# Kernel tuning notes

Measured on AMD Instinct MI355X. Metric: run time of the kernel, lower is better.

The kernel has to match this reference:

```python
import jax, jax.numpy as jnp
import numpy as np

V = 50257      # vocab size
H = 512        # hidden size
S = 128        # source length
BEAM = 5       # beam width (matches beam_width=5 default)
TMAX = 32      # MAX_LENGTH decode cap
SOS, EOS = 1, 2
NEG = -1e9


def setup_inputs() -> dict:
    key = jax.random.key(0)
    ks = jax.random.split(key, 12)
    p = lambda k, shape: jax.random.normal(k, shape, jnp.float32) * 0.02
    return {
        "input_tokens": jax.random.randint(ks[0], (S,), 0, V),
        "embedding": p(ks[1], (V, H)),
        "enc_Wih": p(ks[2], (3 * H, H)),
        "enc_Whh": p(ks[3], (3 * H, H)),
        "enc_bih": jnp.zeros((3 * H,), jnp.float32),
        "enc_bhh": jnp.zeros((3 * H,), jnp.float32),
        "dec_Wih": p(ks[4], (3 * H, H)),
        "dec_Whh": p(ks[5], (3 * H, H)),
        "dec_bih": jnp.zeros((3 * H,), jnp.float32),
        "dec_bhh": jnp.zeros((3 * H,), jnp.float32),
        "W_concat": p(ks[6], (2 * H, H)),
        "W_vocab": p(ks[7], (H, V)),
    }


def gru_cell(x, h, Wih, Whh, bih, bhh):
    # x, h: [..., H]
    gi = x @ Wih.T + bih
    gh = h @ Whh.T + bhh
    ir, iz, inn = jnp.split(gi, 3, -1)
    hr, hz, hn = jnp.split(gh, 3, -1)
    r = jax.nn.sigmoid(ir + hr)
    z = jax.nn.sigmoid(iz + hz)
    n = jnp.tanh(inn + r * hn)
    return (1.0 - z) * n + z * h


def reference(input_tokens, embedding, enc_Wih, enc_Whh, enc_bih, enc_bhh,
              dec_Wih, dec_Whh, dec_bih, dec_bhh, W_concat, W_vocab):
    # ---- encoder: 1-layer GRU over source tokens ----
    src_emb = embedding[input_tokens]                       # [S, H]

    def enc_step(h, x):
        h2 = gru_cell(x, h, enc_Wih, enc_Whh, enc_bih, enc_bhh)
        return h2, h2

    enc_h, enc_out = jax.lax.scan(enc_step, jnp.zeros((H,), src_emb.dtype), src_emb)
    # enc_out: [S, H], enc_h: [H]

    def decode_step(tokens, hidden):
        # tokens: [B] int, hidden: [B, H]
        x = embedding[tokens]                               # [B, H]
        h = gru_cell(x, hidden, dec_Wih, dec_Whh, dec_bih, dec_bhh)
        attn = jax.nn.softmax(h @ enc_out.T, axis=-1)       # [B, S] Luong dot attention
        ctx = attn @ enc_out                                # [B, H]
        o = jnp.tanh(jnp.concatenate([h, ctx], -1) @ W_concat)
        logp = jax.nn.log_softmax(o @ W_vocab, axis=-1)     # [B, V]
        return logp, h

    # ---- batched beam search (GPU-resident equivalent of the heapq loop) ----
    tokens0 = jnp.full((BEAM,), SOS, jnp.int32)
    hidden0 = jnp.tile(enc_h[None], (BEAM, 1))
    scores0 = jnp.full((BEAM,), NEG, jnp.float32).at[0].set(0.0)
    fin0 = jnp.zeros((BEAM,), bool)
    len0 = jnp.ones((BEAM,), jnp.int32)
    seqs0 = jnp.zeros((BEAM, TMAX), jnp.int32)
    fin_row = jnp.full((V,), NEG, jnp.float32).at[EOS].set(0.0)

    def beam_step(state, t):
        tokens, hidden, scores, finished, lengths, seqs = state
        logp, h2 = decode_step(tokens, hidden)              # [BEAM, V]
        step_lp = jnp.where(finished[:, None], fin_row[None, :], logp)
        cand = scores[:, None] + step_lp                    # [BEAM, V]
        top_scores, flat = jax.lax.top_k(cand.reshape(-1), BEAM)
        parent = flat // V
        tok = (flat % V).astype(jnp.int32)
        par_fin = finished[parent]
        new_fin = par_fin | (tok == EOS)
        new_len = lengths[parent] + jnp.where(par_fin, 0, 1)
        new_seqs = seqs[parent].at[:, t].set(jnp.where(par_fin, 0, tok))
        return (tok, h2[parent], top_scores, new_fin, new_len, new_seqs), None

    state, _ = jax.lax.scan(beam_step, (tokens0, hidden0, scores0, fin0, len0, seqs0),
                            jnp.arange(TMAX))
    _, _, scores, _, lengths, seqs = state
    # length-normalized ranking, matching node.logp / node.leng sort
    norm = scores / lengths.astype(scores.dtype)
    order = jnp.argsort(-norm)
    return seqs[order], norm[order]
```

## Files before the change

### kernel.cpp

```cpp
#include <hip/hip_runtime.h>
#include <cstdint>
#include <cstddef>

#define V_SZ 50257
#define H_SZ 512
#define S_SZ 128
#define NBEAM 5
#define TMAXX 32
#define TOK_SOS 1
#define TOK_EOS 2
#define NEGINF (-1e9f)

#define GW 128
#define NT 512
#define GENC 16
#define COLS_PER_WG 393

#define BI_LEAF(l)  ((l)*32)
#define BI_ROOT     256
#define BI_REL(l)   (512 + (l)*32)
#define BI_ECNT     1024
#define BI_EREL     1056

#define OF_GI    0
#define OF_ENC   196608
#define OF_EW    262144
#define OF_H2    327680
#define OF_AL    332800
#define OF_OTOP  333440
#define OF_PV    336000
#define OF_PM    339200
#define OF_PS    339840
#define OF_SC    340480
#define OI_BASE  340488

template <typename T>
__device__ __forceinline__ T aload(const T* p){
  return __hip_atomic_load((T*)p, __ATOMIC_RELAXED, __HIP_MEMORY_SCOPE_AGENT);
}
template <typename T>
__device__ __forceinline__ void astore(T* p, T v){
  __hip_atomic_store(p, v, __ATOMIC_RELAXED, __HIP_MEMORY_SCOPE_AGENT);
}

__device__ __forceinline__ float wredsum(float a){
#pragma unroll
  for (int m = 32; m; m >>= 1) a += __shfl_xor(a, m, 64);
  return a;
}

template <typename F>
__device__ __forceinline__ void dbar(int* bi, int wid, F&& tail){
  __shared__ int s_last;
  int mygen = 0;
  __syncthreads();
  if (threadIdx.x == 0){
    int leaf = wid >> 4;
    mygen = aload(bi + BI_REL(leaf));
    __builtin_amdgcn_s_waitcnt(0);
    int lo = __hip_atomic_fetch_add(bi + BI_LEAF(leaf), 1, __ATOMIC_RELAXED, __HIP_MEMORY_SCOPE_AGENT);
    int last = 0;
    if (lo == 15){
      astore(bi + BI_LEAF(leaf), 0);
      __builtin_amdgcn_s_waitcnt(0);
      int ro = __hip_atomic_fetch_add(bi + BI_ROOT, 1, __ATOMIC_RELAXED, __HIP_MEMORY_SCOPE_AGENT);
      if (ro == (GW/16) - 1){
        astore(bi + BI_ROOT, 0);
        last = 1;
      }
    }
    if (!last){
      while (aload(bi + BI_REL(leaf)) == mygen) __builtin_amdgcn_s_sleep(4);
    }
    s_last = last;
  }
  __syncthreads();
  if (s_last){
    tail();
    __syncthreads();
    if (threadIdx.x == 0){
      __builtin_amdgcn_s_waitcnt(0);
#pragma unroll
      for (int l = 0; l < GW/16; ++l) astore(bi + BI_REL(l), mygen + 1);
    }
  }
  __syncthreads();
}

__global__ __launch_bounds__(256)
void k_gi(const int* __restrict__ toks, const float* __restrict__ emb,
          const float* __restrict__ eWih, const float* __restrict__ ebih,
          float* __restrict__ ws)
{
  float* fb = ws + 2048;
  float* gi = fb + OF_GI;
  const int tid = threadIdx.x, wid = blockIdx.x, lane = tid & 63, wvi = tid >> 6;
  int Wg = wid*4 + wvi;
  for (int it = 0; it < 192; ++it){
    int idx = Wg*192 + it;
    int s = idx / 1536, j = idx - s*1536;
    const float* er = emb + (size_t)toks[s]*H_SZ;
    const float* wr = eWih + (size_t)j*H_SZ;
    float a = 0.f;
#pragma unroll
    for (int u = 0; u < 8; ++u) a += er[u*64+lane]*wr[u*64+lane];
    a = wredsum(a);
    if (lane == 0) gi[idx] = a + ebih[j];
  }
  if (wid == 0){
    float* sc = fb + OF_SC;
    int* ib = (int*)(fb + OI_BASE);
    if (tid < NBEAM){
      sc[tid] = (tid==0) ? 0.f : NEGINF;
      ib[3200+tid] = TOK_SOS; ib[3208+tid] = 0; ib[3216+tid] = 1; ib[3224+tid] = 0;
    }
    for (int q = tid; q < 2*NBEAM*TMAXX; q += 256) ib[3232+q] = 0;
  }
}

__global__ __launch_bounds__(NT, 1)
void k_enc(const float* __restrict__ eWhh, const float* __restrict__ ebhh,
           float* __restrict__ ws)
{
  int* bi = (int*)ws;
  float* fb = ws + 2048;
  float* gi = fb + OF_GI;
  float* enc = fb + OF_ENC;
  const int tid = threadIdx.x, wid = blockIdx.x, lane = tid & 63, wvi = tid >> 6;
  const int i0 = wid*32;
  __shared__ float smF[96];

  float wreg[12][8];
#pragma unroll
  for (int dd = 0; dd < 12; ++dd){
    int d = wvi*12 + dd, g = d >> 5, il = d & 31;
    const float* wr = eWhh + (size_t)(g*512 + i0 + il)*H_SZ;
#pragma unroll
    for (int u = 0; u < 8; ++u) wreg[dd][u] = wr[u*64+lane];
  }

  for (int s = 0; s < S_SZ; ++s){
    float hreg[8];
    if (s == 0){
#pragma unroll
      for (int u = 0; u < 8; ++u) hreg[u] = 0.f;
    } else {
      const float* hp = enc + (size_t)(s-1)*H_SZ;
#pragma unroll
      for (int u = 0; u < 8; ++u) hreg[u] = aload(hp + u*64 + lane);
    }
#pragma unroll
    for (int dd = 0; dd < 12; ++dd){
      float a = 0.f;
#pragma unroll
      for (int u = 0; u < 8; ++u) a += wreg[dd][u]*hreg[u];
      a = wredsum(a);
      if (lane == 0) smF[wvi*12 + dd] = a;
    }
    __syncthreads();
    if (tid < 32){
      int i = i0 + tid;
      float gr = smF[tid], gz = smF[32+tid], gn = smF[64+tid];
      float gir = gi[s*1536 + i], giz = gi[s*1536 + 512 + i], gin = gi[s*1536 + 1024 + i];
      float hprev = (s==0) ? 0.f : aload(enc + (s-1)*H_SZ + i);
      float r = 1.f/(1.f + expf(-(gir + gr + ebhh[i])));
      float z = 1.f/(1.f + expf(-(giz + gz + ebhh[512+i])));
      float n = tanhf(gin + r*(gn + ebhh[1024+i]));
      astore(enc + s*H_SZ + i, (1.f - z)*n + z*hprev);
    }
    __syncthreads();
    if (tid == 0){
      int g = aload(bi + BI_EREL);
      __builtin_amdgcn_s_waitcnt(0);
      int lo = __hip_atomic_fetch_add(bi + BI_ECNT, 1, __ATOMIC_RELAXED, __HIP_MEMORY_SCOPE_AGENT);
      if (lo == GENC - 1){
        astore(bi + BI_ECNT, 0);
        __builtin_amdgcn_s_waitcnt(0);
        astore(bi + BI_EREL, g + 1);
      } else {
        while (aload(bi + BI_EREL) == g) __builtin_amdgcn_s_sleep(2);
      }
    }
    __syncthreads();
  }
}

__global__ __launch_bounds__(NT)
void k_ew(const float* __restrict__ Wc, float* __restrict__ ws)
{
  float* fb = ws + 2048;
  float* enc = fb + OF_ENC;
  float* EW  = fb + OF_EW;
  const int tid = threadIdx.x, wid = blockIdx.x;
  int jc = wid & 15, sb = wid >> 4;
  int jl = tid & 31, sl = (tid >> 5) & 15;
  int s = sb*16 + sl, j = jc*32 + jl;
  const float* er = enc + (size_t)s*H_SZ;
  const float* wc = Wc + (size_t)512*H_SZ;
  float a = 0.f;
  for (int k = 0; k < 512; ++k) a += er[k]*wc[(size_t)k*H_SZ + j];
  EW[s*H_SZ + j] = a;
}

__global__ __launch_bounds__(NT, 1)
void k_dec(const float* __restrict__ emb,
           const float* __restrict__ dWih, const float* __restrict__ dWhh,
           const float* __restrict__ dbih, const float* __restrict__ dbhh,
           const float* __restrict__ Wc,  const float* __restrict__ Wv,
           float* __restrict__ out, float* __restrict__ ws)
{
  const int wid = blockIdx.x, tid = threadIdx.x;
  const int lane = tid & 63, wvi = tid >> 6;
  int* bi = (int*)ws;
  float* fb = ws + 2048;
  float* enc  = fb + OF_ENC;
  float* EW   = fb + OF_EW;
  float* h2   = fb + OF_H2;
  float* al   = fb + OF_AL;
  float* otop = fb + OF_OTOP;
  float* pv   = fb + OF_PV;
  float* pm   = fb + OF_PM;
  float* ps   = fb + OF_PS;
  float* sc   = fb + OF_SC;
  int* ib   = (int*)(fb + OI_BASE);
  int* pidx = ib;
  int* tokA = ib + 3200;
  int* finA = ib + 3208;
  int* lenA = ib + 3216;
  int* parA = ib + 3224;
  int* seqA = ib + 3232;

  __shared__ float smF[1024];
  __shared__ int   smI[256];
  __shared__ float s_buf[2560];
  __shared__ float s_pp[648];

  for (int t = 0; t < TMAXX; ++t){
    float* h2new = h2 + (t & 1)*2560;
    float* h2old = h2 + ((t & 1) ^ 1)*2560;

    if (tid < NBEAM){ smI[tid] = aload(tokA + tid); smI[8 + tid] = t ? aload(parA + tid) : 0; }
    __syncthreads();
    if (t == 0){
      for (int q = tid; q < 2560; q += NT) s_buf[q] = enc[127*H_SZ + (q & 511)];
    } else {
      for (int q = tid; q < 2560; q += NT){
        int b = q >> 9;
        s_buf[q] = aload(h2old + smI[8 + b]*H_SZ + (q & 511));
      }
    }
    __syncthreads();
    {
      int i0 = wid*4;
      int mat = wvi >> 2;
      float srg[5][8];
      if (mat == 0){
#pragma unroll
        for (int b = 0; b < NBEAM; ++b){
          const float* sp = emb + (size_t)smI[b]*H_SZ;
#pragma unroll
          for (int u = 0; u < 8; ++u) srg[b][u] = sp[u*64+lane];
        }
      } else {
#pragma unroll
        for (int b = 0; b < NBEAM; ++b)
#pragma unroll
          for (int u = 0; u < 8; ++u) srg[b][u] = s_buf[b*512 + u*64 + lane];
      }
      for (int rr = 0; rr < 3; ++rr){
        int R = wvi*3 + rr;
        int rem = R - mat*12;
        int g = rem >> 2, il = rem & 3;
        const float* wr = ((mat==0) ? dWih : dWhh) + (size_t)(g*512 + i0 + il)*H_SZ;
        float wreg[8];
#pragma unroll
        for (int u = 0; u < 8; ++u) wreg[u] = wr[u*64+lane];
#pragma unroll
        for (int b = 0; b < NBEAM; ++b){
          float a = 0.f;
#pragma unroll
          for (int u = 0; u < 8; ++u) a += wreg[u]*srg[b][u];
          a = wredsum(a);
          if (lane == 0) smF[R*5 + b] = a;
        }
      }
      __syncthreads();
      if (tid < 20){
        int b = tid >> 2, il = tid & 3;
        int i = i0 + il;
        float ir  = smF[(0*12 + 0*4 + il)*5 + b] + dbih[i];
        float iz  = smF[(0*12 + 1*4 + il)*5 + b] + dbih[512+i];
        float inn = smF[(0*12 + 2*4 + il)*5 + b] + dbih[1024+i];
        float hr  = smF[(1*12 + 0*4 + il)*5 + b] + dbhh[i];
        float hz  = smF[(1*12 + 1*4 + il)*5 + b] + dbhh[512+i];
        float hn  = smF[(1*12 + 2*4 + il)*5 + b] + dbhh[1024+i];
        float r = 1.f/(1.f + expf(-(ir + hr)));
        float z = 1.f/(1.f + expf(-(iz + hz)));
        float n = tanhf(inn + r*hn);
        float hp = s_buf[b*512 + i];
        astore(h2new + b*H_SZ + i, (1.f - z)*n + z*hp);
      }
    }
    dbar(bi, wid, [&](){});

    for (int q = tid; q < 2560; q += NT) s_buf[q] = aload(h2new + q);
    __syncthreads();
    if (wvi < NBEAM){
      const float* er = enc + (size_t)wid*H_SZ;
      float a = 0.f;
#pragma unroll
      for (int u = 0; u < 8; ++u) a += er[u*64+lane]*s_buf[wvi*512 + u*64 + lane];
      a = wredsum(a);
      if (lane == 0) astore(al + wvi*S_SZ + wid, a);
    }
    if (tid < 320){
      int q = tid % 20, ksl = tid / 20;
      int f = wid*20 + q;
      int b = f >> 9, j = f & 511;
      float a = 0.f;
#pragma unroll 8
      for (int u = 0; u < 32; ++u){
        int k = ksl*32 + u;
        a += s_buf[b*512 + k]*Wc[(size_t)k*H_SZ + j];
      }
      smF[q*16 + ksl] = a;
    }
    __syncthreads();
    if (tid < 20){
      float a = 0.f;
#pragma unroll
      for (int u = 0; u < 16; ++u) a += smF[tid*16 + u];
      astore(otop + wid*20 + tid, a);
    }
    dbar(bi, wid, [&](){});

    if (wvi < NBEAM){
      float a1 = aload(al + wvi*S_SZ + lane), a2 = aload(al + wvi*S_SZ + 64 + lane);
      float m = fmaxf(a1, a2);
#pragma unroll
      for (int mm = 32; mm; mm >>= 1) m = fmaxf(m, __shfl_xor(m, mm, 64));
      float e1 = expf(a1 - m), e2 = expf(a2 - m);
      s_pp[wvi*128 + lane] = e1; s_pp[wvi*128 + 64 + lane] = e2;
      float ssv = wredsum(e1 + e2);
      if (lane == 0) s_pp[640 + wvi] = ssv;
    }
    __syncthreads();
    {
      float acc[5] = {0.f,0.f,0.f,0.f,0.f};
      for (int s2 = 0; s2 < 128; ++s2){
        float e = EW[(size_t)s2*H_SZ + tid];
#pragma unroll
        for (int b = 0; b < NBEAM; ++b) acc[b] += e*s_pp[b*128 + s2];
      }
#pragma unroll
      for (int b = 0; b < NBEAM; ++b)
        s_buf[b*512 + tid] = tanhf(aload(otop + b*512 + tid) + acc[b]/s_pp[640 + b]);
    }
    __syncthreads();
    {
      int vbase = wid*COLS_PER_WG;
      int v = vbase + tid;
      bool act = (tid < COLS_PER_WG) && (v < V_SZ);
      int vc = act ? v : vbase;
      const float* wp = Wv + vc;
      float a0=0.f,a1=0.f,a2=0.f,a3=0.f,a4=0.f;
      for (int hb = 0; hb < H_SZ; hb += 16){
        float wr[16];
#pragma unroll
        for (int u = 0; u < 16; ++u) wr[u] = wp[(size_t)(hb+u)*V_SZ];
#pragma unroll
        for (int u = 0; u < 16; ++u){
          float w = wr[u];
          a0 += w*s_buf[hb+u];
          a1 += w*s_buf[512+hb+u];
          a2 += w*s_buf[1024+hb+u];
          a3 += w*s_buf[1536+hb+u];
          a4 += w*s_buf[2048+hb+u];
        }
      }
      if (!act){ a0=a1=a2=a3=a4=-3e38f; }
      int myv = act ? v : 0x7FFFFFFF;
      float accs[5] = {a0,a1,a2,a3,a4};
#pragma unroll
      for (int b = 0; b < NBEAM; ++b){
        float x = accs[b];
        float m = x;
#pragma unroll
        for (int mm = 32; mm; mm >>= 1) m = fmaxf(m, __shfl_xor(m, mm, 64));
        float e = expf(x - m);
        float ssum = wredsum(e);
        float bv = x; int bc = myv;
        float w5[5]; int i5[5];
#pragma unroll
        for (int r = 0; r < 5; ++r){
          float cv2 = bv; int ci2 = bc;
#pragma unroll
          for (int mm = 32; mm; mm >>= 1){
            float ov = __shfl_xor(cv2, mm, 64); int oi = __shfl_xor(ci2, mm, 64);
            bool take = (ov > cv2) || (ov == cv2 && oi < ci2);
            cv2 = take ? ov : cv2; ci2 = take ? oi : ci2;
          }
          w5[r] = cv2; i5[r] = ci2;
          if (bc == ci2) bv = -3e38f;
        }
        if (lane == 0){
#pragma unroll
          for (int r = 0; r < 5; ++r){ smF[(wvi*5+b)*5+r] = w5[r]; smI[(wvi*5+b)*5+r] = i5[r]; }
          smF[300 + wvi*5 + b] = m;
          smF[360 + wvi*5 + b] = ssum;
        }
      }
      __syncthreads();
      if (tid < NBEAM){
        float M = -3.4e38f, Sv = 0.f;
#pragma unroll
        for (int w8 = 0; w8 < 8; ++w8){
          float m2 = smF[300 + w8*5 + tid], s2 = smF[360 + w8*5 + tid];
          if (m2 > M){ Sv = Sv*expf(M - m2) + s2; M = m2; }
          else       { Sv = Sv + s2*expf(m2 - M); }
        }
        astore(pm + wid*5 + tid, M); astore(ps + wid*5 + tid, Sv);
      }
      if (wvi < NBEAM){
        int b = wvi;
        float cval; int cidx;
        if (lane < 40){ cval = smF[((lane/5)*5 + b)*5 + (lane%5)]; cidx = smI[((lane/5)*5 + b)*5 + (lane%5)]; }
        else { cval = -3e38f; cidx = 0x7FFFFFFF; }
        float bv = cval; int bc = cidx;
#pragma unroll
        for (int r = 0; r < 5; ++r){
          float cv2 = bv; int ci2 = bc;
#pragma unroll
          for (int mm = 32; mm; mm >>= 1){
            float ov = __shfl_xor(cv2, mm, 64); int oi = __shfl_xor(ci2, mm, 64);
            bool take = (ov > cv2) || (ov == cv2 && oi < ci2);
            cv2 = take ? ov : cv2; ci2 = take ? oi : ci2;
          }
          if (lane == 0){ astore(pv + (wid*5+b)*5+r, cv2); astore(pidx + (wid*5+b)*5+r, ci2); }
          if (bc == ci2) bv = -3e38f;
        }
      }
    }
    dbar(bi, wid, [&](){
      int b5 = wvi;
      if (b5 < NBEAM){
        float m1 = aload(pm + lane*5 + b5), s1 = aload(ps + lane*5 + b5);
        float m2 = aload(pm + (64+lane)*5 + b5), s2 = aload(ps + (64+lane)*5 + b5);
        float M, Sv;
        if (m1 >= m2){ M = m1; Sv = s1 + s2*expf(m2 - m1); }
        else         { M = m2; Sv = s2 + s1*expf(m1 - m2); }
#pragma unroll
        for (int mm = 32; mm; mm >>= 1){
          float om = __shfl_xor(M, mm, 64), os = __shfl_xor(Sv, mm, 64);
          if (om > M){ Sv = Sv*expf(M - om) + os; M = om; }
          else       { Sv = Sv + os*expf(om - M); }
        }
        if (lane == 0){ smF[8 + b5] = M; smF[80 + b5] = logf(Sv); }
        float lv[5]; int li[5];
#pragma unroll
        for (int r = 0; r < 5; ++r){ lv[r] = aload(pv + (lane*5 + b5)*5 + r); li[r] = aload(pidx + (lane*5 + b5)*5 + r); }
        for (int r = 0; r < 5; ++r){
          float nv = aload(pv + ((64+lane)*5 + b5)*5 + r); int ni = aload(pidx + ((64+lane)*5 + b5)*5 + r);
          bool ins = (nv > lv[4]) || (nv == lv[4] && ni < li[4]);
          if (!ins) break;
          lv[4] = nv; li[4] = ni;
#pragma unroll
          for (int p = 4; p > 0; --p){
            bool sw = (lv[p] > lv[p-1]) || (lv[p] == lv[p-1] && li[p] < li[p-1]);
            if (sw){ float tv = lv[p]; lv[p] = lv[p-1]; lv[p-1] = tv;
                     int ti = li[p]; li[p] = li[p-1]; li[p-1] = ti; }
          }
        }
        float cv = lv[0]; int ci = li[0];
#pragma unroll
        for (int r = 0; r < 5; ++r){
          float xv = cv; int xi = ci;
#pragma unroll
          for (int mm = 32; mm; mm >>= 1){
            float ov = __shfl_xor(xv, mm, 64); int oi = __shfl_xor(xi, mm, 64);
            bool take = (ov > xv) || (ov == xv && oi < xi);
            xv = take ? ov : xv; xi = take ? oi : xi;
          }
          if (lane == 0){ smF[16 + b5*5 + r] = xv; smI[16 + b5*5 + r] = xi; }
          if (ci == xi){
            lv[0]=lv[1]; li[0]=li[1]; lv[1]=lv[2]; li[1]=li[2];
            lv[2]=lv[3]; li[2]=li[3]; lv[3]=lv[4]; li[3]=li[4];
            lv[4] = -3e38f; li[4] = 0x7FFFFFFF;
            cv = lv[0]; ci = li[0];
          }
        }
      }
      __syncthreads();
      if (wvi == 0){
        float cval = -3e38f; int cflat = 0x7FFFFFFF;
        int b = lane/5, k = lane - b*5;
        if (lane < 25){
          if (aload(finA + b)){
            if (k == 0){ cval = aload(sc + b) + 0.0f; cflat = b*V_SZ + TOK_EOS; }
          } else {
            cval = ((smF[16 + b*5 + k] - smF[8 + b]) - smF[80 + b]) + aload(sc + b);
            cflat = b*V_SZ + smI[16 + b*5 + k];
          }
        }
        float bv = cval; int bc = cflat;
#pragma unroll
        for (int r = 0; r < 5; ++r){
          float xv = bv; int xi = bc;
#pragma unroll
          for (int mm = 32; mm; mm >>= 1){
            float ov = __shfl_xor(xv, mm, 64); int oi = __shfl_xor(xi, mm, 64);
            bool take = (ov > xv) || (ov == xv && oi < xi);
            xv = take ? ov : xv; xi = take ? oi : xi;
          }
          if (lane == 0){ smF[48 + r] = xv; smI[48 + r] = xi; }
          if (bc == xi) bv = -3e38f;
        }
        if (lane < NBEAM){
          int r = lane;
          float nscore = smF[48 + r]; int nfl = smI[48 + r];
          int par = nfl / V_SZ; int tok = nfl - par*V_SZ;
          int ofin = aload(finA + par); int olen = aload(lenA + par);
          int nf = (ofin || tok == TOK_EOS) ? 1 : 0;
          int nl = olen + (ofin ? 0 : 1);
          astore(sc + r, nscore); astore(tokA + r, tok); astore(finA + r, nf);
          astore(lenA + r, nl); astore(parA + r, par);
          smI[56 + r] = par; smI[64 + r] = tok; smI[72 + r] = ofin; smI[80 + r] = nl;
          smF[56 + r] = nscore;
        }
      }
      __syncthreads();
      int cur = t & 1, nxt = 1 - cur;
      if (tid < 160){
        int r = tid >> 5, u = tid & 31;
        int par = smI[56 + r];
        int val = aload(seqA + cur*160 + par*32 + u);
        if (u == t) val = smI[72 + r] ? 0 : smI[64 + r];
        astore(seqA + nxt*160 + r*32 + u, val);
      }
      if (t == TMAXX - 1){
        __syncthreads();
        if (tid == 0){
          float nn[5];
#pragma unroll
          for (int r = 0; r < 5; ++r) nn[r] = smF[56 + r] / (float)smI[80 + r];
          int used = 0;
#pragma unroll
          for (int r = 0; r < 5; ++r){
            int best = -1;
            for (int q2 = 0; q2 < 5; ++q2){
              if (used & (1 << q2)) continue;
              if (best < 0 || nn[q2] > nn[best]) best = q2;
            }
            used |= (1 << best);
            smI[88 + r] = best; smF[64 + r] = nn[best];
          }
        }
        __syncthreads();
        if (tid < 160){
          int r = tid >> 5, u = tid & 31;
          int src = smI[88 + r];
          out[tid] = (float)aload(seqA + nxt*160 + src*32 + u);
        }
        if (tid >= 160 && tid < 165) out[tid] = smF[64 + (tid - 160)];
      }
    });
  }
}

extern "C" void kernel_launch(void* const* d_in, const int* in_sizes, int n_in,
                              void* d_out, int out_size, void* d_ws, size_t ws_size,
                              hipStream_t stream)
{
  (void)in_sizes; (void)n_in; (void)out_size; (void)ws_size;
  hipMemsetAsync(d_ws, 0, 8192, stream);
  float* ws = (float*)d_ws;
  k_gi<<<dim3(256), dim3(256), 0, stream>>>(
      (const int*)d_in[0], (const float*)d_in[1],
      (const float*)d_in[2], (const float*)d_in[4], ws);
  k_enc<<<dim3(GENC), dim3(NT), 0, stream>>>(
      (const float*)d_in[3], (const float*)d_in[5], ws);
  k_ew<<<dim3(128), dim3(NT), 0, stream>>>(
      (const float*)d_in[10], ws);
  k_dec<<<dim3(GW), dim3(NT), 0, stream>>>(
      (const float*)d_in[1],
      (const float*)d_in[6], (const float*)d_in[7],
      (const float*)d_in[8], (const float*)d_in[9],
      (const float*)d_in[10], (const float*)d_in[11],
      (float*)d_out, ws);
}
```

Baseline: 3.673 ms.

## Hoist decoder weights into registers, double-buffer vocab loads, relocate sync/workspace offsets

```diff
diff --git a/kernel.cpp b/kernel.cpp
--- a/kernel.cpp
+++ b/kernel.cpp
@@ -17,10 +17,10 @@
 #define COLS_PER_WG 393
 
 #define BI_LEAF(l)  ((l)*32)
-#define BI_ROOT     256
-#define BI_REL(l)   (512 + (l)*32)
-#define BI_ECNT     1024
-#define BI_EREL     1056
+#define BI_ROOT     544
+#define BI_REL(l)   (1024 + (l)*32)
+#define BI_ECNT     1792
+#define BI_EREL     1824
 
 #define OF_GI    0
 #define OF_ENC   196608
@@ -29,10 +29,15 @@
 #define OF_AL    332800
 #define OF_OTOP  333440
 #define OF_PV    336000
-#define OF_PM    339200
-#define OF_PS    339840
-#define OF_SC    340480
-#define OI_BASE  340488
+#define OF_PM    342400
+#define OF_PS    343680
+#define OF_SC    344960
+#define OI_BASE  344968
+#define I_TOK 6400
+#define I_FIN 6408
+#define I_LEN 6416
+#define I_PAR 6424
+#define I_SEQ 6432
 
 template <typename T>
 __device__ __forceinline__ T aload(const T* p){
@@ -112,9 +117,9 @@
     int* ib = (int*)(fb + OI_BASE);
     if (tid < NBEAM){
       sc[tid] = (tid==0) ? 0.f : NEGINF;
-      ib[3200+tid] = TOK_SOS; ib[3208+tid] = 0; ib[3216+tid] = 1; ib[3224+tid] = 0;
-    }
-    for (int q = tid; q < 2*NBEAM*TMAXX; q += 256) ib[3232+q] = 0;
+      ib[I_TOK+tid] = TOK_SOS; ib[I_FIN+tid] = 0; ib[I_LEN+tid] = 1; ib[I_PAR+tid] = 0;
+    }
+    for (int q = tid; q < 2*NBEAM*TMAXX; q += 256) ib[I_SEQ+q] = 0;
   }
 }
 
@@ -138,6 +143,11 @@
 #pragma unroll
     for (int u = 0; u < 8; ++u) wreg[dd][u] = wr[u*64+lane];
   }
+  float eb0 = 0.f, eb1 = 0.f, eb2 = 0.f;
+  if (tid < 32){
+    int i = i0 + tid;
+    eb0 = ebhh[i]; eb1 = ebhh[512+i]; eb2 = ebhh[1024+i];
+  }
 
   for (int s = 0; s < S_SZ; ++s){
     float hreg[8];
@@ -163,9 +173,9 @@
       float gr = smF[tid], gz = smF[32+tid], gn = smF[64+tid];
       float gir = gi[s*1536 + i], giz = gi[s*1536 + 512 + i], gin = gi[s*1536 + 1024 + i];
       float hprev = (s==0) ? 0.f : aload(enc + (s-1)*H_SZ + i);
-      float r = 1.f/(1.f + expf(-(gir + gr + ebhh[i])));
-      float z = 1.f/(1.f + expf(-(giz + gz + ebhh[512+i])));
-      float n = tanhf(gin + r*(gn + ebhh[1024+i]));
+      float r = 1.f/(1.f + expf(-(gir + gr + eb0)));
+      float z = 1.f/(1.f + expf(-(giz + gz + eb1)));
+      float n = tanhf(gin + r*(gn + eb2));
       astore(enc + s*H_SZ + i, (1.f - z)*n + z*hprev);
     }
     __syncthreads();
@@ -202,7 +212,7 @@
   EW[s*H_SZ + j] = a;
 }
 
-__global__ __launch_bounds__(NT, 1)
+__global__ __launch_bounds__(NT, 2)
 void k_dec(const float* __restrict__ emb,
            const float* __restrict__ dWih, const float* __restrict__ dWhh,
            const float* __restrict__ dbih, const float* __restrict__ dbhh,
@@ -224,16 +234,44 @@
   float* sc   = fb + OF_SC;
   int* ib   = (int*)(fb + OI_BASE);
   int* pidx = ib;
-  int* tokA = ib + 3200;
-  int* finA = ib + 3208;
-  int* lenA = ib + 3216;
-  int* parA = ib + 3224;
-  int* seqA = ib + 3232;
-
-  __shared__ float smF[1024];
+  int* tokA = ib + I_TOK;
+  int* finA = ib + I_FIN;
+  int* lenA = ib + I_LEN;
+  int* parA = ib + I_PAR;
+  int* seqA = ib + I_SEQ;
+
+  __shared__ float smF[512];
   __shared__ int   smI[256];
   __shared__ float s_buf[2560];
   __shared__ float s_pp[648];
+
+  const int i0 = wid*4;
+  const int mat = wvi >> 2;
+  float wreg3[3][8];
+#pragma unroll
+  for (int rr = 0; rr < 3; ++rr){
+    int R = wvi*3 + rr;
+    int rem = R - mat*12;
+    int g = rem >> 2, il = rem & 3;
+    const float* wr = ((mat==0) ? dWih : dWhh) + (size_t)(g*512 + i0 + il)*H_SZ;
+#pragma unroll
+    for (int u = 0; u < 8; ++u) wreg3[rr][u] = wr[u*64+lane];
+  }
+  float pbih0=0.f,pbih1=0.f,pbih2=0.f,pbhh0=0.f,pbhh1=0.f,pbhh2=0.f;
+  if (tid < 20){
+    int i = i0 + (tid & 3);
+    pbih0 = dbih[i]; pbih1 = dbih[512+i]; pbih2 = dbih[1024+i];
+    pbhh0 = dbhh[i]; pbhh1 = dbhh[512+i]; pbhh2 = dbhh[1024+i];
+  }
+  const int bq   = tid % 20;
+  const int bksl = tid / 20;
+  const int bf   = wid*20 + bq;
+  const int bb   = bf >> 9, bj = bf & 511;
+  float wcreg[32];
+  if (tid < 320){
+#pragma unroll
+    for (int u = 0; u < 32; ++u) wcreg[u] = Wc[(size_t)(bksl*32 + u)*H_SZ + bj];
+  }
 
   for (int t = 0; t < TMAXX; ++t){
     float* h2new = h2 + (t & 1)*2560;
@@ -251,8 +289,6 @@
     }
     __syncthreads();
     {
-      int i0 = wid*4;
-      int mat = wvi >> 2;
       float srg[5][8];
       if (mat == 0){
 #pragma unroll
@@ -267,19 +303,14 @@
 #pragma unroll
           for (int u = 0; u < 8; ++u) srg[b][u] = s_buf[b*512 + u*64 + lane];
       }
+#pragma unroll
       for (int rr = 0; rr < 3; ++rr){
         int R = wvi*3 + rr;
-        int rem = R - mat*12;
-        int g = rem >> 2, il = rem & 3;
-        const float* wr = ((mat==0) ? dWih : dWhh) + (size_t)(g*512 + i0 + il)*H_SZ;
-        float wreg[8];
-#pragma unroll
-        for (int u = 0; u < 8; ++u) wreg[u] = wr[u*64+lane];
 #pragma unroll
         for (int b = 0; b < NBEAM; ++b){
           float a = 0.f;
 #pragma unroll
-          for (int u = 0; u < 8; ++u) a += wreg[u]*srg[b][u];
+          for (int u = 0; u < 8; ++u) a += wreg3[rr][u]*srg[b][u];
           a = wredsum(a);
           if (lane == 0) smF[R*5 + b] = a;
         }
@@ -288,12 +319,12 @@
       if (tid < 20){
         int b = tid >> 2, il = tid & 3;
         int i = i0 + il;
-        float ir  = smF[(0*12 + 0*4 + il)*5 + b] + dbih[i];
-        float iz  = smF[(0*12 + 1*4 + il)*5 + b] + dbih[512+i];
-        float inn = smF[(0*12 + 2*4 + il)*5 + b] + dbih[1024+i];
-        float hr  = smF[(1*12 + 0*4 + il)*5 + b] + dbhh[i];
-        float hz  = smF[(1*12 + 1*4 + il)*5 + b] + dbhh[512+i];
-        float hn  = smF[(1*12 + 2*4 + il)*5 + b] + dbhh[1024+i];
+        float ir  = smF[(0*12 + 0*4 + il)*5 + b] + pbih0;
+        float iz  = smF[(0*12 + 1*4 + il)*5 + b] + pbih1;
+        float inn = smF[(0*12 + 2*4 + il)*5 + b] + pbih2;
+        float hr  = smF[(1*12 + 0*4 + il)*5 + b] + pbhh0;
+        float hz  = smF[(1*12 + 1*4 + il)*5 + b] + pbhh1;
+        float hn  = smF[(1*12 + 2*4 + il)*5 + b] + pbhh2;
         float r = 1.f/(1.f + expf(-(ir + hr)));
         float z = 1.f/(1.f + expf(-(iz + hz)));
         float n = tanhf(inn + r*hn);
@@ -314,16 +345,10 @@
       if (lane == 0) astore(al + wvi*S_SZ + wid, a);
     }
     if (tid < 320){
-      int q = tid % 20, ksl = tid / 20;
-      int f = wid*20 + q;
-      int b = f >> 9, j = f & 511;
       float a = 0.f;
-#pragma unroll 8
-      for (int u = 0; u < 32; ++u){
-        int k = ksl*32 + u;
-        a += s_buf[b*512 + k]*Wc[(size_t)k*H_SZ + j];
-      }
-      smF[q*16 + ksl] = a;
+#pragma unroll
+      for (int u = 0; u < 32; ++u) a += s_buf[bb*512 + bksl*32 + u]*wcreg[u];
+      smF[bq*16 + bksl] = a;
     }
     __syncthreads();
     if (tid < 20){
@@ -364,18 +389,33 @@
       int vc = act ? v : vbase;
       const float* wp = Wv + vc;
       float a0=0.f,a1=0.f,a2=0.f,a3=0.f,a4=0.f;
-      for (int hb = 0; hb < H_SZ; hb += 16){
-        float wr[16];
-#pragma unroll
-        for (int u = 0; u < 16; ++u) wr[u] = wp[(size_t)(hb+u)*V_SZ];
-#pragma unroll
-        for (int u = 0; u < 16; ++u){
-          float w = wr[u];
-          a0 += w*s_buf[hb+u];
-          a1 += w*s_buf[512+hb+u];
-          a2 += w*s_buf[1024+hb+u];
-          a3 += w*s_buf[1536+hb+u];
-          a4 += w*s_buf[2048+hb+u];
+      float wrA[32], wrB[32];
+#pragma unroll
+      for (int u = 0; u < 32; ++u) wrA[u] = wp[(size_t)u*V_SZ];
+      for (int hb = 0; hb < 512; hb += 64){
+#pragma unroll
+        for (int u = 0; u < 32; ++u) wrB[u] = wp[(size_t)(hb+32+u)*V_SZ];
+#pragma unroll
+        for (int u = 0; u < 32; ++u){
+          float w = wrA[u]; int h = hb + u;
+          a0 += w*s_buf[h];
+          a1 += w*s_buf[512+h];
+          a2 += w*s_buf[1024+h];
+          a3 += w*s_buf[1536+h];
+          a4 += w*s_buf[2048+h];
+        }
+        if (hb + 64 < 512){
+#pragma unroll
+          for (int u = 0; u < 32; ++u) wrA[u] = wp[(size_t)(hb+64+u)*V_SZ];
+        }
+#pragma unroll
+        for (int u = 0; u < 32; ++u){
+          float w = wrB[u]; int h = hb + 32 + u;
+          a0 += w*s_buf[h];
+          a1 += w*s_buf[512+h];
+          a2 += w*s_buf[1024+h];
+          a3 += w*s_buf[1536+h];
+          a4 += w*s_buf[2048+h];
         }
       }
       if (!act){ a0=a1=a2=a3=a4=-3e38f; }
@@ -457,13 +497,16 @@
         }
         if (lane == 0){ smF[8 + b5] = M; smF[80 + b5] = logf(Sv); }
         float lv[5]; int li[5];
-#pragma unroll
-        for (int r = 0; r < 5; ++r){ lv[r] = aload(pv + (lane*5 + b5)*5 + r); li[r] = aload(pidx + (lane*5 + b5)*5 + r); }
+        float nv5[5]; int ni5[5];
+#pragma unroll
         for (int r = 0; r < 5; ++r){
-          float nv = aload(pv + ((64+lane)*5 + b5)*5 + r); int ni = aload(pidx + ((64+lane)*5 + b5)*5 + r);
-          bool ins = (nv > lv[4]) || (nv == lv[4] && ni < li[4]);
+          lv[r]  = aload(pv + (lane*5 + b5)*5 + r);      li[r]  = aload(pidx + (lane*5 + b5)*5 + r);
+          nv5[r] = aload(pv + ((64+lane)*5 + b5)*5 + r); ni5[r] = aload(pidx + ((64+lane)*5 + b5)*5 + r);
+        }
+        for (int r = 0; r < 5; ++r){
+          bool ins = (nv5[r] > lv[4]) || (nv5[r] == lv[4] && ni5[r] < li[4]);
           if (!ins) break;
-          lv[4] = nv; li[4] = ni;
+          lv[4] = nv5[r]; li[4] = ni5[r];
 #pragma unroll
           for (int p = 4; p > 0; --p){
             bool sw = (lv[p] > lv[p-1]) || (lv[p] == lv[p-1] && li[p] < li[p-1]);
```

After: 6.462 ms. +75.9%, slower.
